# Kernel tuning notes

Hardware: AMD Instinct MI355X
Metric: run time of the kernel (lower is better)

The kernel has to match this reference:

```python
import jax, jax.numpy as jnp
import numpy as np

K = 5          # window_size
PAD = K // 2

def _unfold(t):
    # torch.nn.functional.unfold(t, K, stride=1, padding=PAD)
    # t: [B,C,H,W] -> [B, C*K*K, H*W], patch index flattened channel-major (c, ki, kj)
    B, C, H, W = t.shape
    tp = jnp.pad(t, ((0, 0), (0, 0), (PAD, PAD), (PAD, PAD)))
    cols = jnp.stack([tp[:, :, i:i + H, j:j + W] for i in range(K) for j in range(K)], axis=2)  # [B,C,K*K,H,W]
    return cols.reshape(B, C * K * K, H * W)

def _fold(cols, H, W):
    # torch.nn.functional.fold(cols, (H,W), K, padding=PAD): overlap-add inverse of unfold
    B, CKK, _ = cols.shape
    C = CKK // (K * K)
    c = cols.reshape(B, C, K, K, H, W)
    outp = jnp.zeros((B, C, H + 2 * PAD, W + 2 * PAD), dtype=cols.dtype)
    for i in range(K):
        for j in range(K):
            outp = outp.at[:, :, i:i + H, j:j + W].add(c[:, :, i, j])
    return outp[:, :, PAD:PAD + H, PAD:PAD + W]

def setup_inputs() -> dict:
    key = jax.random.key(0)
    ks = jax.random.split(key, 8)
    C = 64
    x = jax.random.normal(ks[0], (4, 128, 128, C), dtype=jnp.float32)
    Wq = jax.random.normal(ks[1], (C // 8, C), dtype=jnp.float32) * 0.1
    bq = jax.random.normal(ks[2], (C // 8,), dtype=jnp.float32) * 0.1
    Wk = jax.random.normal(ks[3], (C // 8, C), dtype=jnp.float32) * 0.1
    bk = jax.random.normal(ks[4], (C // 8,), dtype=jnp.float32) * 0.1
    Wv = jax.random.normal(ks[5], (C, C), dtype=jnp.float32) * 0.1
    bv = jax.random.normal(ks[6], (C,), dtype=jnp.float32) * 0.1
    gamma = jax.random.normal(ks[7], (1,), dtype=jnp.float32)
    return {"x": x, "Wq": Wq, "bq": bq, "Wk": Wk, "bk": bk, "Wv": Wv, "bv": bv, "gamma": gamma}

def reference(x, Wq, bq, Wk, bk, Wv, bv, gamma):
    # channels_last input -> NCHW
    xc = jnp.transpose(x, (0, 3, 1, 2))
    B, C, H, W = xc.shape
    pdim = K * K
    # 1x1 convs == per-pixel linear
    q = jnp.einsum('bchw,oc->bohw', xc, Wq) + bq[None, :, None, None]
    k = jnp.einsum('bchw,oc->bohw', xc, Wk) + bk[None, :, None, None]
    v = jnp.einsum('bchw,oc->bohw', xc, Wv) + bv[None, :, None, None]
    # unfold then the module's raw (patch_dim, C) reinterpretation reshape
    qp = _unfold(q).transpose(0, 2, 1).reshape(B, H, W, pdim, -1)
    kp = _unfold(k).transpose(0, 2, 1).reshape(B, H, W, pdim, -1)
    vp = _unfold(v).transpose(0, 2, 1).reshape(B, H, W, pdim, -1)
    logits = jnp.einsum('bhwnc,bhwmc->bhwnm', qp, kp)
    attn = jax.nn.softmax(logits, axis=-1)
    local = jnp.einsum('bhwnm,bhwmc->bhwnc', attn, vp)  # [B,H,W,25,C]
    cols = local.reshape(B, H * W, -1).transpose(0, 2, 1)  # raw reinterpretation back to fold layout
    folded = _fold(cols, H, W)
    out = gamma[0] * folded + xc
    out = jnp.transpose(out, (0, 2, 3, 1))  # back to channels_last
    return out, attn
```

## Files before the change

### kernel.cpp

```cpp
#include <hip/hip_runtime.h>
#include <hip/hip_fp16.h>

#define NPIX (4*128*128)
#define OUT_ELEMS (NPIX*64)

typedef _Float16 half8 __attribute__((ext_vector_type(8)));
typedef float f32x16 __attribute__((ext_vector_type(16)));

__device__ __forceinline__ int div25(int v) { return (v * 5243) >> 17; }
__device__ __forceinline__ int div5(int v)  { return (v * 205) >> 10; }

__global__ __launch_bounds__(256) void k1_qkv(
    const float* __restrict__ x,
    const float* __restrict__ Wq, const float* __restrict__ bq,
    const float* __restrict__ Wk, const float* __restrict__ bk,
    const float* __restrict__ Wv, const float* __restrict__ bv,
    float* __restrict__ qws, float* __restrict__ kws, float* __restrict__ vws,
    float* __restrict__ out_init)
{
    __shared__ float sWv[64 * 65];
    __shared__ float sWqk[16 * 65];

    int t = threadIdx.x;
    for (int e = t; e < 64 * 64; e += 256) sWv[(e >> 6) * 65 + (e & 63)] = Wv[e];
    for (int e = t; e < 8 * 64; e += 256) {
        int o = e >> 6, c = e & 63;
        sWqk[o * 65 + c]       = Wq[e];
        sWqk[(o + 8) * 65 + c] = Wk[e];
    }
    __syncthreads();

    int wid = t >> 6, lane = t & 63;
    bool isq = lane < 8;
    bool isk = (lane >= 8) && (lane < 16);
    const float* wr  = sWv + lane * 65;
    const float* wr2 = sWqk + (lane & 7) * 65 + (isk ? 8 * 65 : 0);
    float bvl = bv[lane];
    float bql = isq ? bq[lane] : (isk ? bk[lane - 8] : 0.f);

    #pragma unroll 1
    for (int i = 0; i < 8; ++i) {
        int pix = blockIdx.x * 32 + wid * 8 + i;
        float xv = x[(size_t)pix * 64 + lane];
        float accv = bvl, accq = bql;
        #pragma unroll
        for (int cc = 0; cc < 64; ++cc) {
            float xc = __shfl(xv, cc);
            accv = fmaf(xc, wr[cc], accv);
            accq = fmaf(xc, wr2[cc], accq);
        }
        vws[(size_t)pix * 64 + lane] = accv;
        if (out_init) out_init[(size_t)pix * 64 + lane] = xv;
        if (isq)      qws[(size_t)pix * 8 + lane] = accq;
        else if (isk) kws[(size_t)pix * 8 + (lane - 8)] = accq;
    }
}

__global__ __launch_bounds__(128) void k2_attn_ws(
    const float* __restrict__ qws, const float* __restrict__ kws,
    const float* __restrict__ vws,
    float* __restrict__ attn, __half* __restrict__ lws)
{
    __shared__ float smem[2 * 1764];

    int tid = threadIdx.x, wid = tid >> 6, lane = tid & 63;
    float* W   = smem + wid * 1764;
    float* Qs  = W;
    float* E   = W + 204;
    float* R   = W + 932;
    __half* Vth = (__half*)(W + 964);
    __half* LBh = Vth;

    int pix = blockIdx.x * 2 + wid;
    int b = pix >> 14, y = (pix >> 7) & 127, x = pix & 127;
    size_t ibase = (size_t)b << 14;

    if (lane < 25) {
        float* er = E + lane * 28;
        er[25] = 0.f; er[26] = 0.f; er[27] = 0.f;
    }
    if (lane < 28) E[700 + lane] = 0.f;

    const float* vb = vws + ibase * 64;
    int vbase = lane * 25;
    #pragma unroll
    for (int p = 0; p < 25; ++p) {
        int i5 = div5(p);
        int yy = y + i5 - 2, xx = x + (p - i5 * 5) - 2;
        float val = 0.f;
        if ((unsigned)yy < 128u && (unsigned)xx < 128u)
            val = vb[(size_t)(((yy << 7) + xx) * 64 + lane)];
        Vth[vbase + p] = __float2half(val);
    }

    const float* qb = qws + ibase * 8;
    const float* kb = kws + ibase * 8;
    #pragma unroll
    for (int i = 0; i < 4; ++i) {
        int e = lane + (i << 6);
        if (e < 200) {
            int cq = div25(e), p = e - cq * 25;
            int i5 = div5(p);
            int yy = y + i5 - 2, xx = x + (p - i5 * 5) - 2;
            float qv = 0.f;
            if ((unsigned)yy < 128u && (unsigned)xx < 128u)
                qv = qb[((yy << 7) + xx) * 8 + cq];
            Qs[e] = qv;
        }
    }

    {
        bool act = lane < 50;
        int m_l = (lane < 25) ? lane : (act ? lane - 25 : 0);
        int n0  = (lane < 25) ? 0 : 13;
        float kreg[8];
        #pragma unroll
        for (int cc = 0; cc < 8; ++cc) {
            int g  = m_l * 8 + cc;
            int cv = div25(g), p = g - cv * 25;
            int i5 = div5(p);
            int yy = y + i5 - 2, xx = x + (p - i5 * 5) - 2;
            float kv = 0.f;
            if (act && (unsigned)yy < 128u && (unsigned)xx < 128u)
                kv = kb[((yy << 7) + xx) * 8 + cv];
            kreg[cc] = kv;
        }
        #pragma unroll
        for (int t = 0; t < 13; ++t) {
            int n = n0 + t;
            bool ok = act && (n < 25);
            int nn = ok ? n : 0;
            const float4* qr = (const float4*)(Qs + (nn << 3));
            float4 q0 = qr[0], q1 = qr[1];
            float s = q0.x * kreg[0] + q0.y * kreg[1] + q0.z * kreg[2] + q0.w * kreg[3]
                    + q1.x * kreg[4] + q1.y * kreg[5] + q1.z * kreg[6] + q1.w * kreg[7];
            if (ok) E[n * 28 + m_l] = s;
        }
    }

    if (lane < 50) {
        int n = lane >> 1, hf = lane & 1;
        float* row = E + n * 28;
        int m0 = hf * 12;
        float mx = -3.4e38f;
        #pragma unroll
        for (int t = 0; t < 13; ++t) mx = fmaxf(mx, row[m0 + t]);
        mx = fmaxf(mx, __shfl_xor(mx, 1));
        float sum = 0.f;
        #pragma unroll
        for (int t = 0; t < 13; ++t) {
            int m = m0 + t;
            float ev = __expf(row[m] - mx);
            row[m] = ev;
            sum += (hf && t == 0) ? 0.f : ev;
        }
        sum += __shfl_xor(sum, 1);
        R[n] = 1.f / sum;
    }

    float* ab = attn + (size_t)pix * 625;
    #pragma unroll
    for (int i = 0; i < 10; ++i) {
        int e = lane + (i << 6);
        if (e < 625) {
            int n = div25(e), m = e - n * 25;
            ab[e] = E[n * 28 + m] * R[n];
        }
    }

    int h  = lane >> 5;
    int lo = lane & 31;

    half8 afr[2];
    #pragma unroll
    for (int s = 0; s < 2; ++s) {
        const float4* ep = (const float4*)(E + lo * 28 + 16 * s + 8 * h);
        float4 p0 = ep[0], p1 = ep[1];
        afr[s][0] = (_Float16)p0.x; afr[s][1] = (_Float16)p0.y;
        afr[s][2] = (_Float16)p0.z; afr[s][3] = (_Float16)p0.w;
        afr[s][4] = (_Float16)p1.x; afr[s][5] = (_Float16)p1.y;
        afr[s][6] = (_Float16)p1.z; afr[s][7] = (_Float16)p1.w;
    }

    f32x16 acc0 = {0,0,0,0,0,0,0,0,0,0,0,0,0,0,0,0};
    f32x16 acc1 = {0,0,0,0,0,0,0,0,0,0,0,0,0,0,0,0};
    #pragma unroll
    for (int s = 0; s < 2; ++s) {
        half8 b0, b1;
        #pragma unroll
        for (int j = 0; j < 8; ++j) {
            int k = 16 * s + 8 * h + j;
            bool ok = (k < 25);
            int off = ok ? (((16 * s + j) << 6) + (h << 9)) : 0;
            _Float16 v0 = Vth[off + lo];
            _Float16 v1 = Vth[off + 32 + lo];
            b0[j] = ok ? v0 : (_Float16)0.f;
            b1[j] = ok ? v1 : (_Float16)0.f;
        }
        acc0 = __builtin_amdgcn_mfma_f32_32x32x16_f16(afr[s], b0, acc0, 0, 0, 0);
        acc1 = __builtin_amdgcn_mfma_f32_32x32x16_f16(afr[s], b1, acc1, 0, 0, 0);
    }

    #pragma unroll
    for (int r16 = 0; r16 < 16; ++r16) {
        int row = (r16 & 3) + 8 * (r16 >> 2) + 4 * h;
        if (row < 25) {
            float rn = R[row];
            LBh[(row << 6) + lo]      = __float2half(acc0[r16] * rn);
            LBh[(row << 6) + 32 + lo] = __float2half(acc1[r16] * rn);
        }
    }

    #pragma unroll
    for (int p = 0; p < 25; ++p)
        lws[((size_t)p * NPIX + (size_t)pix) * 64 + lane] = LBh[lane * 25 + p];
}

__global__ __launch_bounds__(256) void k3_fold(
    const float* __restrict__ x, const __half* __restrict__ lws,
    const float* __restrict__ gamma, float* __restrict__ out)
{
    int tid = threadIdx.x, wid = tid >> 6, lane = tid & 63;
    int pix4 = (blockIdx.x * 4 + wid) * 4;
    int b = pix4 >> 14, y = (pix4 >> 7) & 127, x0 = pix4 & 127;
    int sub = lane >> 4;
    int ch4 = (lane & 15) << 2;
    size_t ibase = (size_t)b << 14;

    float s0 = 0.f, s1 = 0.f, s2 = 0.f, s3 = 0.f;
    #pragma unroll
    for (int i = 0; i < 5; ++i) {
        int cy = y + 2 - i;
        if ((unsigned)cy >= 128u) continue;
        #pragma unroll
        for (int j = 0; j < 5; ++j) {
            int cx = x0 + sub + 2 - j;
            if ((unsigned)cx < 128u) {
                size_t src = ((size_t)(i * 5 + j) * NPIX + (ibase + (size_t)((cy << 7) + cx))) * 64 + ch4;
                float2 w = *(const float2*)(lws + src);
                __half2 h0 = *(__half2*)&w.x, h1 = *(__half2*)&w.y;
                float2 fa = __half22float2(h0), fb = __half22float2(h1);
                s0 += fa.x; s1 += fa.y; s2 += fb.x; s3 += fb.y;
            }
        }
    }

    float g = gamma[0];
    size_t o = ((size_t)pix4 + sub) * 64 + ch4;
    float4 xv = *(const float4*)(x + o);
    float4 r;
    r.x = fmaf(g, s0, xv.x);
    r.y = fmaf(g, s1, xv.y);
    r.z = fmaf(g, s2, xv.z);
    r.w = fmaf(g, s3, xv.w);
    *(float4*)(out + o) = r;
}

__device__ __forceinline__ void attn_core_fb(
    int lane, int y, int x, size_t ibase,
    const float* __restrict__ qws, const float* __restrict__ kws,
    const float* __restrict__ vws, float* __restrict__ attn,
    float* V, float* Qs, float* Ks, float* E, float* R, float vr[25])
{
    const float* vb = vws + ibase * 64;
    #pragma unroll
    for (int p = 0; p < 25; ++p) {
        int i5 = div5(p);
        int yy = y + i5 - 2, xx = x + (p - i5 * 5) - 2;
        float val = 0.f;
        if ((unsigned)yy < 128u && (unsigned)xx < 128u)
            val = vb[(size_t)(((yy << 7) + xx) * 64 + lane)];
        V[p * 65 + lane] = val;
    }
    const float* qb = qws + ibase * 8;
    const float* kb = kws + ibase * 8;
    #pragma unroll
    for (int i = 0; i < 4; ++i) {
        int e = lane + (i << 6);
        if (e < 200) {
            int cq = div25(e), p = e - cq * 25;
            int i5 = div5(p);
            int yy = y + i5 - 2, xx = x + (p - i5 * 5) - 2;
            float qv = 0.f, kv = 0.f;
            if ((unsigned)yy < 128u && (unsigned)xx < 128u) {
                int off = ((yy << 7) + xx) * 8 + cq;
                qv = qb[off];
                kv = kb[off];
            }
            Qs[e] = qv;
            Ks[e] = kv;
        }
    }
    #pragma unroll
    for (int m = 0; m < 25; ++m) {
        int g = (m << 6) + lane;
        int cv = div25(g), p = g - cv * 25;
        vr[m] = V[p * 65 + cv];
    }
    #pragma unroll
    for (int i = 0; i < 10; ++i) {
        int e = lane + (i << 6);
        if (e < 625) {
            int n = div25(e), m = e - n * 25;
            const float4* qr = (const float4*)(Qs + (n << 3));
            const float4* kr = (const float4*)(Ks + (m << 3));
            float4 q0 = qr[0], q1 = qr[1], k0 = kr[0], k1 = kr[1];
            E[n * 28 + m] = q0.x * k0.x + q0.y * k0.y + q0.z * k0.z + q0.w * k0.w
                          + q1.x * k1.x + q1.y * k1.y + q1.z * k1.z + q1.w * k1.w;
        }
    }
    if (lane < 25) {
        float* row = E + lane * 28;
        float mx = -3.4e38f;
        #pragma unroll
        for (int m = 0; m < 25; ++m) mx = fmaxf(mx, row[m]);
        float s = 0.f;
        #pragma unroll
        for (int m = 0; m < 25; ++m) {
            float ev = __expf(row[m] - mx);
            row[m] = ev;
            s += ev;
        }
        R[lane] = 1.f / s;
    }
    float* ab = attn + (ibase + (size_t)((y << 7) + x)) * 625;
    #pragma unroll
    for (int i = 0; i < 10; ++i) {
        int e = lane + (i << 6);
        if (e < 625) {
            int n = div25(e), m = e - n * 25;
            ab[e] = E[n * 28 + m] * R[n];
        }
    }
}

__global__ __launch_bounds__(256) void k2_attn_atomic(
    const float* __restrict__ qws, const float* __restrict__ kws,
    const float* __restrict__ vws, const float* __restrict__ gamma,
    float* __restrict__ out, float* __restrict__ attn)
{
    __shared__ float sV[4][1632];
    __shared__ float sQ[4][200];
    __shared__ float sK[4][200];
    __shared__ float sE[4][704];
    __shared__ float sR[4][32];

    int tid = threadIdx.x, wid = tid >> 6, lane = tid & 63;
    int pix = blockIdx.x * 4 + wid;
    int b = pix >> 14, y = (pix >> 7) & 127, x = pix & 127;
    size_t ibase = (size_t)b << 14;

    float vr[25];
    attn_core_fb(lane, y, x, ibase, qws, kws, vws, attn,
                 sV[wid], sQ[wid], sK[wid], sE[wid], sR[wid], vr);

    float g0 = gamma[0];
    float acc[25];
    float* E = sE[wid];
    float* R = sR[wid];
    #pragma unroll
    for (int n = 0; n < 25; ++n) {
        const float4* er = (const float4*)(E + n * 28);
        float aa = E[n * 28 + 24] * vr[24];
        #pragma unroll
        for (int q4 = 0; q4 < 6; ++q4) {
            float4 ev = er[q4];
            aa = fmaf(ev.x, vr[q4 * 4 + 0], aa);
            aa = fmaf(ev.y, vr[q4 * 4 + 1], aa);
            aa = fmaf(ev.z, vr[q4 * 4 + 2], aa);
            aa = fmaf(ev.w, vr[q4 * 4 + 3], aa);
        }
        acc[n] = aa * (R[n] * g0);
    }

    float* LB = sV[wid];
    #pragma unroll
    for (int n = 0; n < 25; ++n) LB[(n << 6) + lane] = acc[n];

    float* ob = out + ibase * 64;
    #pragma unroll
    for (int p = 0; p < 25; ++p) {
        int i5 = div5(p);
        int ty = y + i5 - 2, tx = x + (p - i5 * 5) - 2;
        if ((unsigned)ty < 128u && (unsigned)tx < 128u)
            atomicAdd(ob + (size_t)(((ty << 7) + tx) * 64 + lane), LB[lane * 25 + p]);
    }
}

extern "C" void kernel_launch(void* const* d_in, const int* in_sizes, int n_in,
                              void* d_out, int out_size, void* d_ws, size_t ws_size,
                              hipStream_t stream)
{
    const float* x  = (const float*)d_in[0];
    const float* Wq = (const float*)d_in[1];
    const float* bq = (const float*)d_in[2];
    const float* Wk = (const float*)d_in[3];
    const float* bk = (const float*)d_in[4];
    const float* Wv = (const float*)d_in[5];
    const float* bv = (const float*)d_in[6];
    const float* gm = (const float*)d_in[7];

    float* out  = (float*)d_out;
    float* attn = out + OUT_ELEMS;

    float* qws = (float*)d_ws;
    float* kws = qws + (size_t)NPIX * 8;
    float* vws = kws + (size_t)NPIX * 8;
    __half* lws = (__half*)(vws + (size_t)NPIX * 64);

    const size_t need = (size_t)NPIX * 80 * 4 + (size_t)NPIX * 1600 * 2;

    if (ws_size >= need) {
        hipLaunchKernelGGL(k1_qkv, dim3(NPIX / 32), dim3(256), 0, stream,
                           x, Wq, bq, Wk, bk, Wv, bv, qws, kws, vws, (float*)nullptr);
        hipLaunchKernelGGL(k2_attn_ws, dim3(NPIX / 2), dim3(128), 0, stream,
                           qws, kws, vws, attn, lws);
        hipLaunchKernelGGL(k3_fold, dim3(NPIX / 16), dim3(256), 0, stream,
                           x, lws, gm, out);
    } else {
        hipLaunchKernelGGL(k1_qkv, dim3(NPIX / 32), dim3(256), 0, stream,
                           x, Wq, bq, Wk, bk, Wv, bv, qws, kws, vws, out);
        hipLaunchKernelGGL(k2_attn_atomic, dim3(NPIX / 4), dim3(256), 0, stream,
                           qws, kws, vws, gm, out, attn);
    }
}
```

Measured before the change: 288.2 us.

## Split attention kernel into logits/softmax and PV kernels

The fused attention kernel is split into two kernels. The first computes logits and softmax and writes normalized attention. The second re-reads that attention from global memory, converts it to half, and runs the MFMA P·V product. The aim is lower shared-memory and register use per kernel so more waves fit per CU, with 4 pixels per block instead of 2. The cost is an extra launch and an extra global round trip of the 625-float attention per pixel (about 164 MB read).

New measurement: 329.3 us. +14.3%, slower.

```diff
diff --git a/kernel.cpp b/kernel.cpp
--- a/kernel.cpp
+++ b/kernel.cpp
@@ -56,42 +56,21 @@
     }
 }
 
-__global__ __launch_bounds__(128) void k2_attn_ws(
+__global__ __launch_bounds__(256) void k2a_logits(
     const float* __restrict__ qws, const float* __restrict__ kws,
-    const float* __restrict__ vws,
-    float* __restrict__ attn, __half* __restrict__ lws)
-{
-    __shared__ float smem[2 * 1764];
+    float* __restrict__ attn)
+{
+    __shared__ float smem[4 * 964];
 
     int tid = threadIdx.x, wid = tid >> 6, lane = tid & 63;
-    float* W   = smem + wid * 1764;
-    float* Qs  = W;
-    float* E   = W + 204;
-    float* R   = W + 932;
-    __half* Vth = (__half*)(W + 964);
-    __half* LBh = Vth;
-
-    int pix = blockIdx.x * 2 + wid;
+    float* W  = smem + wid * 964;
+    float* Qs = W;
+    float* E  = W + 204;
+    float* R  = W + 932;
+
+    int pix = blockIdx.x * 4 + wid;
     int b = pix >> 14, y = (pix >> 7) & 127, x = pix & 127;
     size_t ibase = (size_t)b << 14;
-
-    if (lane < 25) {
-        float* er = E + lane * 28;
-        er[25] = 0.f; er[26] = 0.f; er[27] = 0.f;
-    }
-    if (lane < 28) E[700 + lane] = 0.f;
-
-    const float* vb = vws + ibase * 64;
-    int vbase = lane * 25;
-    #pragma unroll
-    for (int p = 0; p < 25; ++p) {
-        int i5 = div5(p);
-        int yy = y + i5 - 2, xx = x + (p - i5 * 5) - 2;
-        float val = 0.f;
-        if ((unsigned)yy < 128u && (unsigned)xx < 128u)
-            val = vb[(size_t)(((yy << 7) + xx) * 64 + lane)];
-        Vth[vbase + p] = __float2half(val);
-    }
 
     const float* qb = qws + ibase * 8;
     const float* kb = kws + ibase * 8;
@@ -167,20 +146,60 @@
             ab[e] = E[n * 28 + m] * R[n];
         }
     }
+}
+
+__global__ __launch_bounds__(256) void k2b_pv(
+    const float* __restrict__ vws, const float* __restrict__ attn,
+    __half* __restrict__ lws)
+{
+    __shared__ __half smem2[4 * 2336];
+
+    int tid = threadIdx.x, wid = tid >> 6, lane = tid & 63;
+    __half* Vth = smem2 + wid * 2336;
+    __half* LBh = Vth;
+    __half* Eh  = Vth + 1600;
+
+    int pix = blockIdx.x * 4 + wid;
+    int b = pix >> 14, y = (pix >> 7) & 127, x = pix & 127;
+    size_t ibase = (size_t)b << 14;
+
+    if (lane < 25) {
+        __half* er = Eh + lane * 28;
+        __half z = __float2half(0.f);
+        er[25] = z; er[26] = z; er[27] = z;
+    }
+    if (lane < 28) Eh[700 + lane] = __float2half(0.f);
+
+    const float* vb = vws + ibase * 64;
+    int vbase = lane * 25;
+    #pragma unroll
+    for (int p = 0; p < 25; ++p) {
+        int i5 = div5(p);
+        int yy = y + i5 - 2, xx = x + (p - i5 * 5) - 2;
+        float val = 0.f;
+        if ((unsigned)yy < 128u && (unsigned)xx < 128u)
+            val = vb[(size_t)(((yy << 7) + xx) * 64 + lane)];
+        Vth[vbase + p] = __float2half(val);
+    }
+
+    const float* ab = attn + (size_t)pix * 625;
+    #pragma unroll
+    for (int i = 0; i < 10; ++i) {
+        int e = lane + (i << 6);
+        if (e < 625) {
+            int n = div25(e), m = e - n * 25;
+            Eh[n * 28 + m] = __float2half(ab[e]);
+        }
+    }
 
     int h  = lane >> 5;
     int lo = lane & 31;
+    int arow = (lo < 26) ? lo : 0;
 
     half8 afr[2];
     #pragma unroll
-    for (int s = 0; s < 2; ++s) {
-        const float4* ep = (const float4*)(E + lo * 28 + 16 * s + 8 * h);
-        float4 p0 = ep[0], p1 = ep[1];
-        afr[s][0] = (_Float16)p0.x; afr[s][1] = (_Float16)p0.y;
-        afr[s][2] = (_Float16)p0.z; afr[s][3] = (_Float16)p0.w;
-        afr[s][4] = (_Float16)p1.x; afr[s][5] = (_Float16)p1.y;
-        afr[s][6] = (_Float16)p1.z; afr[s][7] = (_Float16)p1.w;
-    }
+    for (int s = 0; s < 2; ++s)
+        afr[s] = *(const half8*)(Eh + arow * 28 + 16 * s + 8 * h);
 
     f32x16 acc0 = {0,0,0,0,0,0,0,0,0,0,0,0,0,0,0,0};
     f32x16 acc1 = {0,0,0,0,0,0,0,0,0,0,0,0,0,0,0,0};
@@ -205,9 +224,8 @@
     for (int r16 = 0; r16 < 16; ++r16) {
         int row = (r16 & 3) + 8 * (r16 >> 2) + 4 * h;
         if (row < 25) {
-            float rn = R[row];
-            LBh[(row << 6) + lo]      = __float2half(acc0[r16] * rn);
-            LBh[(row << 6) + 32 + lo] = __float2half(acc1[r16] * rn);
+            LBh[(row << 6) + lo]      = __float2half(acc0[r16]);
+            LBh[(row << 6) + 32 + lo] = __float2half(acc1[r16]);
         }
     }
 
@@ -413,8 +431,10 @@
     if (ws_size >= need) {
         hipLaunchKernelGGL(k1_qkv, dim3(NPIX / 32), dim3(256), 0, stream,
                            x, Wq, bq, Wk, bk, Wv, bv, qws, kws, vws, (float*)nullptr);
-        hipLaunchKernelGGL(k2_attn_ws, dim3(NPIX / 2), dim3(128), 0, stream,
-                           qws, kws, vws, attn, lws);
+        hipLaunchKernelGGL(k2a_logits, dim3(NPIX / 4), dim3(256), 0, stream,
+                           qws, kws, attn);
+        hipLaunchKernelGGL(k2b_pv, dim3(NPIX / 4), dim3(256), 0, stream,
+                           vws, attn, lws);
         hipLaunchKernelGGL(k3_fold, dim3(NPIX / 16), dim3(256), 0, stream,
                            x, lws, gm, out);
     } else {
```
